# Optimization experiments

Hardware: AMD Instinct MI355X
Metric: run time of the kernel (lower is better)

Reference implementation:

```python
import jax, jax.numpy as jnp
import numpy as np

N_CLASSES = 100
EPSILON = 1e-07


def setup_inputs() -> dict:
    key = jax.random.key(0)
    k1, k2 = jax.random.split(key)
    y_pred = jax.random.normal(k1, (2000000, N_CLASSES), dtype=jnp.float32)
    y_true = jax.random.randint(k2, (2000000,), 0, N_CLASSES, dtype=jnp.int64)
    return {"y_pred": y_pred, "y_true": y_true}


def reference(y_pred, y_true):
    C = N_CLASSES
    pred = jnp.argmax(y_pred, axis=1)  # [N]
    # confusion matrix: rows = true class, cols = predicted class
    flat_idx = y_true.astype(jnp.int32) * C + pred.astype(jnp.int32)
    conf = jnp.zeros((C * C,), dtype=y_pred.dtype).at[flat_idx].add(1.0).reshape(C, C)
    TP = jnp.diag(conf)                      # [C]
    col_sum = jnp.sum(conf, axis=0)          # [C] sum over rows for each predicted label
    FN = col_sum - TP                        # original: conf[idx!=label, label].sum()
    sensitivity = jnp.sum(TP / (TP + FN + EPSILON)) / C
    return sensitivity
```

## Files before the change

kernel.cpp:

```cpp
#include <hip/hip_runtime.h>
#include <stdint.h>

#define N_CLASSES 100
#define ROWS_PER_WTILE 16
#define DW_PER_WTILE (ROWS_PER_WTILE * N_CLASSES)
#define LOADS_PER_LANE (DW_PER_WTILE / 64)
#define BLOCK 256
#define WAVES_PER_BLOCK (BLOCK / 64)
#define EPS 1e-7f

__device__ __forceinline__ void lds_dma4(void* lds, const void* g) {
    __builtin_amdgcn_global_load_lds(
        (const __attribute__((address_space(1))) uint32_t*)g,
        (__attribute__((address_space(3))) uint32_t*)lds, 4, 0, 0);
}

__global__ __launch_bounds__(BLOCK) void sens_count_kernel(
    const float* __restrict__ y_pred, const int* __restrict__ y_true,
    unsigned int* __restrict__ counters, int n_rows)
{
    __shared__ float s_rows[WAVES_PER_BLOCK][2][DW_PER_WTILE];
    __shared__ unsigned int s_pc[N_CLASSES];
    __shared__ unsigned int s_tp[N_CLASSES];

    const int tid  = threadIdx.x;
    const int wave = tid >> 6;
    const int lane = tid & 63;

    for (int i = tid; i < N_CLASSES; i += BLOCK) { s_pc[i] = 0u; s_tp[i] = 0u; }
    __syncthreads();

    const long long n_wtiles = ((long long)n_rows + ROWS_PER_WTILE - 1) / ROWS_PER_WTILE;
    const long long total_dw = (long long)n_rows * N_CLASSES;
    const long long stride   = (long long)gridDim.x * WAVES_PER_BLOCK;

    auto issue = [&](long long t, int b) {
        const long long base = t * (long long)DW_PER_WTILE;
        float* dst = s_rows[wave][b];
        const float* gp = y_pred + base;
        if (base + DW_PER_WTILE <= total_dw) {
            #pragma unroll
            for (int k = 0; k < LOADS_PER_LANE; ++k) {
                const int i = k * 64 + lane;
                lds_dma4(dst + i, gp + i);
            }
        } else {
            #pragma unroll
            for (int k = 0; k < LOADS_PER_LANE; ++k) {
                const int i = k * 64 + lane;
                long long gi = base + i;
                if (gi >= total_dw) gi = total_dw - 1;
                lds_dma4(dst + i, y_pred + gi);
            }
        }
    };

    long long t = (long long)blockIdx.x * WAVES_PER_BLOCK + wave;
    int cur = 0;
    if (t < n_wtiles) issue(t, 0);

    for (; t < n_wtiles; t += stride) {
        const int r = lane >> 2;
        const int q = lane & 3;
        const long long grow = t * ROWS_PER_WTILE + r;

        int tv = -1;
        if (grow < (long long)n_rows) tv = y_true[grow];

        const long long nxt = t + stride;
        if (nxt < n_wtiles) {
            issue(nxt, cur ^ 1);
            asm volatile("s_waitcnt vmcnt(25)" ::: "memory");
        } else {
            asm volatile("s_waitcnt vmcnt(0)" ::: "memory");
        }

        if (grow < (long long)n_rows) {
            const float* rowp = &s_rows[wave][cur][r * N_CLASSES + q * 25];
            float best = rowp[0];
            int bidx = q * 25;
            #pragma unroll
            for (int i2 = 1; i2 < 25; ++i2) {
                float v = rowp[i2];
                if (v > best) { best = v; bidx = q * 25 + i2; }
            }
            #pragma unroll
            for (int m = 1; m <= 2; m <<= 1) {
                float ov = __shfl_xor(best, m, 64);
                int   oi = __shfl_xor(bidx, m, 64);
                if (ov > best || (ov == best && oi < bidx)) { best = ov; bidx = oi; }
            }
            if (q == 0) {
                atomicAdd(&s_pc[bidx], 1u);
                if (tv == bidx) atomicAdd(&s_tp[bidx], 1u);
            }
        }
        cur ^= 1;
    }

    __syncthreads();
    for (int i = tid; i < N_CLASSES; i += BLOCK) {
        unsigned int pc = s_pc[i], tp = s_tp[i];
        if (pc) atomicAdd(&counters[i], pc);
        if (tp) atomicAdd(&counters[N_CLASSES + i], tp);
    }
}

__global__ void sens_final_kernel(const unsigned int* __restrict__ counters,
                                  float* __restrict__ out)
{
    const int lane = threadIdx.x;
    float acc = 0.f;
    for (int c = lane; c < N_CLASSES; c += 64) {
        float pc = (float)counters[c];
        float tp = (float)counters[N_CLASSES + c];
        acc += tp / (pc + EPS);
    }
    #pragma unroll
    for (int m = 32; m >= 1; m >>= 1) acc += __shfl_xor(acc, m, 64);
    if (lane == 0) out[0] = acc / (float)N_CLASSES;
}

extern "C" void kernel_launch(void* const* d_in, const int* in_sizes, int n_in,
                              void* d_out, int out_size, void* d_ws, size_t ws_size,
                              hipStream_t stream)
{
    const float* y_pred = (const float*)d_in[0];
    const int*   y_true = (const int*)d_in[1];
    float* out = (float*)d_out;
    const int n_rows = in_sizes[1];

    unsigned int* counters = (unsigned int*)d_ws;
    hipMemsetAsync(counters, 0, 2 * N_CLASSES * sizeof(unsigned int), stream);

    const int grid = 768;
    sens_count_kernel<<<grid, BLOCK, 0, stream>>>(y_pred, y_true, counters, n_rows);
    sens_final_kernel<<<1, 64, 0, stream>>>(counters, out);
}
```

Measured before the change: 148.4 us.

## Use 16-byte LDS DMA loads and fuse final reduction via last-block pattern

Switches the global-to-LDS DMA from 25 dword loads per lane to six 16-byte loads plus one dword load, which cuts the number of memory instructions per tile. The main loop is restructured so the y_true load is issued with inline asm and the wait is tightened to vmcnt(7), with a sched barrier keeping the compute after the wait. The separate finalize kernel is removed: the last block to finish, found with an atomic ticket counter, computes the final sensitivity. This saves a kernel launch but adds a fence and atomic at the end of every block.

```diff
diff --git a/kernel.cpp b/kernel.cpp
--- a/kernel.cpp
+++ b/kernel.cpp
@@ -4,24 +4,30 @@
 #define N_CLASSES 100
 #define ROWS_PER_WTILE 16
 #define DW_PER_WTILE (ROWS_PER_WTILE * N_CLASSES)
-#define LOADS_PER_LANE (DW_PER_WTILE / 64)
 #define BLOCK 256
 #define WAVES_PER_BLOCK (BLOCK / 64)
+#define GRID 768
 #define EPS 1e-7f
 
+__device__ __forceinline__ void lds_dma16(void* lds, const void* g) {
+    __builtin_amdgcn_global_load_lds(
+        (const __attribute__((address_space(1))) uint32_t*)g,
+        (__attribute__((address_space(3))) uint32_t*)lds, 16, 0, 0);
+}
 __device__ __forceinline__ void lds_dma4(void* lds, const void* g) {
     __builtin_amdgcn_global_load_lds(
         (const __attribute__((address_space(1))) uint32_t*)g,
         (__attribute__((address_space(3))) uint32_t*)lds, 4, 0, 0);
 }
 
-__global__ __launch_bounds__(BLOCK) void sens_count_kernel(
+__global__ __launch_bounds__(BLOCK) void sens_kernel(
     const float* __restrict__ y_pred, const int* __restrict__ y_true,
-    unsigned int* __restrict__ counters, int n_rows)
+    unsigned int* __restrict__ counters, float* __restrict__ out, int n_rows)
 {
     __shared__ float s_rows[WAVES_PER_BLOCK][2][DW_PER_WTILE];
     __shared__ unsigned int s_pc[N_CLASSES];
     __shared__ unsigned int s_tp[N_CLASSES];
+    __shared__ int s_last;
 
     const int tid  = threadIdx.x;
     const int wave = tid >> 6;
@@ -34,49 +40,35 @@
     const long long total_dw = (long long)n_rows * N_CLASSES;
     const long long stride   = (long long)gridDim.x * WAVES_PER_BLOCK;
 
-    auto issue = [&](long long t, int b) {
-        const long long base = t * (long long)DW_PER_WTILE;
+    auto issue = [&](long long tt, int b) {
+        const long long base_dw = tt * (long long)DW_PER_WTILE;
         float* dst = s_rows[wave][b];
-        const float* gp = y_pred + base;
-        if (base + DW_PER_WTILE <= total_dw) {
+        const float* gp = y_pred + base_dw;
+        if (base_dw + DW_PER_WTILE <= total_dw) {
             #pragma unroll
-            for (int k = 0; k < LOADS_PER_LANE; ++k) {
-                const int i = k * 64 + lane;
-                lds_dma4(dst + i, gp + i);
+            for (int k = 0; k < 6; ++k) {
+                const int i = (k * 64 + lane) * 4;
+                lds_dma16(dst + i, gp + i);
             }
+            const int j = 6 * 64 * 4 + lane;
+            lds_dma4(dst + j, gp + j);
         } else {
             #pragma unroll
-            for (int k = 0; k < LOADS_PER_LANE; ++k) {
+            for (int k = 0; k < 25; ++k) {
                 const int i = k * 64 + lane;
-                long long gi = base + i;
+                long long gi = base_dw + i;
                 if (gi >= total_dw) gi = total_dw - 1;
                 lds_dma4(dst + i, y_pred + gi);
             }
         }
     };
 
-    long long t = (long long)blockIdx.x * WAVES_PER_BLOCK + wave;
-    int cur = 0;
-    if (t < n_wtiles) issue(t, 0);
-
-    for (; t < n_wtiles; t += stride) {
+    auto compute = [&](long long tt, int b, int tv) {
         const int r = lane >> 2;
         const int q = lane & 3;
-        const long long grow = t * ROWS_PER_WTILE + r;
-
-        int tv = -1;
-        if (grow < (long long)n_rows) tv = y_true[grow];
-
-        const long long nxt = t + stride;
-        if (nxt < n_wtiles) {
-            issue(nxt, cur ^ 1);
-            asm volatile("s_waitcnt vmcnt(25)" ::: "memory");
-        } else {
-            asm volatile("s_waitcnt vmcnt(0)" ::: "memory");
-        }
-
+        const long long grow = tt * ROWS_PER_WTILE + r;
         if (grow < (long long)n_rows) {
-            const float* rowp = &s_rows[wave][cur][r * N_CLASSES + q * 25];
+            const float* rowp = &s_rows[wave][b][r * N_CLASSES + q * 25];
             float best = rowp[0];
             int bidx = q * 25;
             #pragma unroll
@@ -95,7 +87,34 @@
                 if (tv == bidx) atomicAdd(&s_tp[bidx], 1u);
             }
         }
-        cur ^= 1;
+    };
+
+    long long t = (long long)blockIdx.x * WAVES_PER_BLOCK + wave;
+    int cur = 0;
+    if (t < n_wtiles) {
+        issue(t, 0);
+        long long nxt = t + stride;
+        while (nxt < n_wtiles) {
+            int tv;
+            const int* typ = y_true + t * ROWS_PER_WTILE + (lane >> 2);
+            asm volatile("global_load_dword %0, %1, off"
+                         : "=v"(tv) : "v"(typ) : "memory");
+            issue(nxt, cur ^ 1);
+            asm volatile("s_waitcnt vmcnt(7)" ::: "memory");
+            __builtin_amdgcn_sched_barrier(0);
+            compute(t, cur, tv);
+            cur ^= 1;
+            t = nxt;
+            nxt += stride;
+        }
+        {
+            const long long grow = t * ROWS_PER_WTILE + (lane >> 2);
+            int tv = -1;
+            if (grow < (long long)n_rows) tv = y_true[grow];
+            asm volatile("s_waitcnt vmcnt(0)" ::: "memory");
+            __builtin_amdgcn_sched_barrier(0);
+            compute(t, cur, tv);
+        }
     }
 
     __syncthreads();
@@ -104,21 +123,28 @@
         if (pc) atomicAdd(&counters[i], pc);
         if (tp) atomicAdd(&counters[N_CLASSES + i], tp);
     }
-}
+    __threadfence();
+    __syncthreads();
+    if (tid == 0) {
+        unsigned int old = atomicAdd(&counters[2 * N_CLASSES], 1u);
+        s_last = (old == (unsigned int)(gridDim.x - 1)) ? 1 : 0;
+    }
+    __syncthreads();
 
-__global__ void sens_final_kernel(const unsigned int* __restrict__ counters,
-                                  float* __restrict__ out)
-{
-    const int lane = threadIdx.x;
-    float acc = 0.f;
-    for (int c = lane; c < N_CLASSES; c += 64) {
-        float pc = (float)counters[c];
-        float tp = (float)counters[N_CLASSES + c];
-        acc += tp / (pc + EPS);
+    if (s_last && tid < 64) {
+        __threadfence();
+        float acc = 0.f;
+        for (int c = tid; c < N_CLASSES; c += 64) {
+            unsigned int pc = __hip_atomic_load(&counters[c],
+                                __ATOMIC_RELAXED, __HIP_MEMORY_SCOPE_AGENT);
+            unsigned int tp = __hip_atomic_load(&counters[N_CLASSES + c],
+                                __ATOMIC_RELAXED, __HIP_MEMORY_SCOPE_AGENT);
+            acc += (float)tp / ((float)pc + EPS);
+        }
+        #pragma unroll
+        for (int m = 32; m >= 1; m >>= 1) acc += __shfl_xor(acc, m, 64);
+        if (tid == 0) out[0] = acc / (float)N_CLASSES;
     }
-    #pragma unroll
-    for (int m = 32; m >= 1; m >>= 1) acc += __shfl_xor(acc, m, 64);
-    if (lane == 0) out[0] = acc / (float)N_CLASSES;
 }
 
 extern "C" void kernel_launch(void* const* d_in, const int* in_sizes, int n_in,
@@ -131,9 +157,7 @@
     const int n_rows = in_sizes[1];
 
     unsigned int* counters = (unsigned int*)d_ws;
-    hipMemsetAsync(counters, 0, 2 * N_CLASSES * sizeof(unsigned int), stream);
+    hipMemsetAsync(counters, 0, (2 * N_CLASSES + 1) * sizeof(unsigned int), stream);
 
-    const int grid = 768;
-    sens_count_kernel<<<grid, BLOCK, 0, stream>>>(y_pred, y_true, counters, n_rows);
-    sens_final_kernel<<<1, 64, 0, stream>>>(counters, out);
+    sens_kernel<<<GRID, BLOCK, 0, stream>>>(y_pred, y_true, counters, out, n_rows);
 }
```

Result: slower. 227.3 us (+53.1%).
